# Kernel optimization log

Measured on AMD Instinct MI355X. Metric: run time of the kernel, lower is better.

The kernel has to match this reference:

```python
import jax, jax.numpy as jnp
import numpy as np

NUM_HEADS = 8
NUM_GROUPS = 32
EPS = 1e-5


def setup_inputs() -> dict:
    key = jax.random.key(0)
    ks = jax.random.split(key, 7)
    B, C, H, W = 8, 512, 32, 32
    x = jax.random.normal(ks[0], (B, C, H, W), dtype=jnp.float32)
    # GroupNorm affine params
    gn_w = jnp.ones((C,), dtype=jnp.float32)
    gn_b = jnp.zeros((C,), dtype=jnp.float32)
    # 1x1 conv == linear over channel dim; store squeezed weights (out, in)
    qkv_w = jax.random.normal(ks[1], (3 * C, C), dtype=jnp.float32) * (1.0 / np.sqrt(C))
    qkv_b = jnp.zeros((3 * C,), dtype=jnp.float32)
    proj_w = jax.random.normal(ks[2], (C, C), dtype=jnp.float32) * (1.0 / np.sqrt(C))
    proj_b = jnp.zeros((C,), dtype=jnp.float32)
    return {"x": x, "gn_w": gn_w, "gn_b": gn_b, "qkv_w": qkv_w,
            "qkv_b": qkv_b, "proj_w": proj_w, "proj_b": proj_b}


def reference(x, gn_w, gn_b, qkv_w, qkv_b, proj_w, proj_b):
    B, C, H, W = x.shape
    G = NUM_GROUPS
    hd = C // NUM_HEADS
    scale = hd ** -0.5
    # GroupNorm: normalize over (C//G, H, W) per group
    xg = x.reshape(B, G, C // G, H, W)
    mean = xg.mean(axis=(2, 3, 4), keepdims=True)
    var = xg.var(axis=(2, 3, 4), keepdims=True)
    xn = ((xg - mean) * jax.lax.rsqrt(var + EPS)).reshape(B, C, H, W)
    xn = xn * gn_w[None, :, None, None] + gn_b[None, :, None, None]
    # QKV 1x1 conv
    qkv = jnp.einsum('bchw,oc->bohw', xn, qkv_w) + qkv_b[None, :, None, None]
    # (B, 3, heads, head_dim, HW) -> (3, B, heads, HW, head_dim)
    qkv = qkv.reshape(B, 3, NUM_HEADS, hd, H * W).transpose(1, 0, 2, 4, 3)
    q, k, v = qkv[0], qkv[1], qkv[2]
    attn = jax.nn.softmax(jnp.einsum('bhqd,bhkd->bhqk', q, k) * scale, axis=-1)
    out = jnp.einsum('bhqk,bhkd->bhqd', attn, v)  # (B, heads, HW, hd)
    out = out.transpose(0, 1, 3, 2).reshape(B, C, H, W)
    out = jnp.einsum('bchw,oc->bohw', out, proj_w) + proj_b[None, :, None, None]
    return out + x
```

## Files before the change

kernel.cpp:

```cpp
#include <hip/hip_runtime.h>
#include <hip/hip_bf16.h>
#include <math.h>

typedef __bf16 bf16_t;
typedef __bf16 bf16x8 __attribute__((ext_vector_type(8)));
typedef __bf16 bf16x4 __attribute__((ext_vector_type(4)));
typedef float  f32x4  __attribute__((ext_vector_type(4)));
typedef short  short4v __attribute__((ext_vector_type(4)));

#define NB    8
#define NC    512
#define NHW   1024
#define NHEAD 8
#define NHD   64
#define NG    32
#define NCG   16
#define NO3   1536
#define KVB   64
#define NKT   16

__device__ __forceinline__ void lds_load16(bf16_t* lds, const bf16_t* g) {
  __builtin_amdgcn_global_load_lds(
      (__attribute__((address_space(1))) unsigned int*)(g),
      (__attribute__((address_space(3))) unsigned int*)(void*)(lds),
      16, 0, 0);
}

__device__ __forceinline__ f32x4 mfma16(bf16x4 a, bf16x4 b, f32x4 c) {
#if __has_builtin(__builtin_amdgcn_mfma_f32_16x16x16bf16_1k)
  return __builtin_amdgcn_mfma_f32_16x16x16bf16_1k(
      __builtin_bit_cast(short4v, a), __builtin_bit_cast(short4v, b), c, 0, 0, 0);
#else
  f32x4 d;
  asm("v_mfma_f32_16x16x16_bf16 %0, %1, %2, %3"
      : "=v"(d) : "v"(a), "v"(b), "v"(c));
  return d;
#endif
}

__device__ __forceinline__ float fexp2(float x) {
#if __has_builtin(__builtin_amdgcn_exp2f)
  return __builtin_amdgcn_exp2f(x);
#else
  return exp2f(x);
#endif
}

__global__ __launch_bounds__(256)
void gnw_kernel(const float* __restrict__ x, const float* __restrict__ gw,
                const float* __restrict__ gb, bf16_t* __restrict__ xn,
                const float* __restrict__ qw, const float* __restrict__ pw,
                bf16_t* __restrict__ qwb, bf16_t* __restrict__ pwb)
{
  const int bid = blockIdx.x;
  const int tid = threadIdx.x;

  if (bid >= NB * NG) {
    const int gid = (bid - NB * NG) * 256 + tid;
    const int n1 = NO3 * NC / 4;
    float4 v; bf16x4 o;
    if (gid < n1) {
      v = ((const float4*)qw)[gid];
      o[0] = (bf16_t)v.x; o[1] = (bf16_t)v.y; o[2] = (bf16_t)v.z; o[3] = (bf16_t)v.w;
      ((bf16x4*)qwb)[gid] = o;
    } else {
      int g2 = gid - n1;
      v = ((const float4*)pw)[g2];
      o[0] = (bf16_t)v.x; o[1] = (bf16_t)v.y; o[2] = (bf16_t)v.z; o[3] = (bf16_t)v.w;
      ((bf16x4*)pwb)[g2] = o;
    }
    return;
  }

  const int b = bid >> 5, g = bid & 31;
  const float* xp = x + ((size_t)b * NC + g * NCG) * NHW;
  const int wave = tid >> 6, lane = tid & 63;

  float4 v[16];
  const float4* xp4 = (const float4*)xp;
  float s1 = 0.f, s2 = 0.f;
  #pragma unroll
  for (int c = 0; c < 16; ++c) {
    v[c] = xp4[c * 256 + tid];
    s1 += v[c].x + v[c].y + v[c].z + v[c].w;
    s2 += v[c].x * v[c].x + v[c].y * v[c].y + v[c].z * v[c].z + v[c].w * v[c].w;
  }
  for (int off = 32; off > 0; off >>= 1) {
    s1 += __shfl_down(s1, off);
    s2 += __shfl_down(s2, off);
  }
  __shared__ float red[16];
  if (lane == 0) { red[wave] = s1; red[8 + wave] = s2; }
  __syncthreads();
  float tot1 = red[0] + red[1] + red[2] + red[3];
  float tot2 = red[8] + red[9] + red[10] + red[11];
  const float mean = tot1 * (1.0f / 16384.0f);
  const float var  = tot2 * (1.0f / 16384.0f) - mean * mean;
  const float rstd = rsqrtf(var + 1e-5f);

  float gam[NCG], bet[NCG];
  #pragma unroll
  for (int c = 0; c < NCG; ++c) {
    gam[c] = gw[g * NCG + c] * rstd;
    bet[c] = gb[g * NCG + c] - mean * gam[c];
  }
  bf16_t* op = xn + (size_t)b * NHW * NC + g * NCG;
  #pragma unroll
  for (int jj = 0; jj < 4; ++jj) {
    int s = 4 * tid + jj;
    __align__(16) bf16_t vals[NCG];
    #pragma unroll
    for (int c = 0; c < NCG; ++c) {
      float xv = (jj == 0) ? v[c].x : (jj == 1) ? v[c].y : (jj == 2) ? v[c].z : v[c].w;
      vals[c] = (bf16_t)(xv * gam[c] + bet[c]);
    }
    *(bf16x8*)(op + (size_t)s * NC)     = *(const bf16x8*)&vals[0];
    *(bf16x8*)(op + (size_t)s * NC + 8) = *(const bf16x8*)&vals[8];
  }
}

__global__ __launch_bounds__(256, 2)
void qkv_gemm(const bf16_t* __restrict__ xn, const bf16_t* __restrict__ w,
              const float* __restrict__ bias,
              bf16_t* __restrict__ qbuf, bf16_t* __restrict__ kbuf, bf16_t* __restrict__ vbuf)
{
  __shared__ __align__(16) char smem[65536];
  const int tid = threadIdx.x;
  const int wave = tid >> 6, lane = tid & 63;
  const int quad = lane >> 4, l16 = lane & 15;
  const int wm = wave >> 1, wn = wave & 1;
  const int bx = blockIdx.x, by = blockIdx.y, b = blockIdx.z;

  const bf16_t* Ap = xn + ((size_t)b * NHW + by * 128) * NC;
  const bf16_t* Bp = w + (size_t)bx * 128 * NC;

  auto stage = [&](int k0, int bufi) {
    bf16_t* sA = (bf16_t*)(smem + bufi * 32768);
    bf16_t* sB = (bf16_t*)(smem + bufi * 32768 + 16384);
    #pragma unroll
    for (int j = 0; j < 4; ++j) {
      int c = wave * 64 + j * 256 + lane;
      int row = c >> 3, ko = ((c ^ (c >> 3)) & 7) * 8;
      lds_load16(sA + (size_t)(wave * 64 + j * 256) * 8, Ap + (size_t)row * 512 + k0 + ko);
      lds_load16(sB + (size_t)(wave * 64 + j * 256) * 8, Bp + (size_t)row * 512 + k0 + ko);
    }
  };

  f32x4 acc[4][4] = {};
  stage(0, 0);
  __syncthreads();
  const int swr = (l16 & 7) << 4;
  for (int t = 0; t < 8; ++t) {
    const int cur = t & 1;
    if (t < 7) stage((t + 1) * 64, cur ^ 1);
    const char* sA = smem + cur * 32768;
    const char* sB = sA + 16384;
    #pragma unroll
    for (int kc = 0; kc < 2; ++kc) {
      bf16x8 af[4], bfr[4];
      #pragma unroll
      for (int mi = 0; mi < 4; ++mi)
        af[mi] = *(const bf16x8*)(sA + (wm * 64 + mi * 16 + l16) * 128 + ((kc * 64 + quad * 16) ^ swr));
      #pragma unroll
      for (int ni = 0; ni < 4; ++ni)
        bfr[ni] = *(const bf16x8*)(sB + (wn * 64 + ni * 16 + l16) * 128 + ((kc * 64 + quad * 16) ^ swr));
      #pragma unroll
      for (int mi = 0; mi < 4; ++mi)
        #pragma unroll
        for (int ni = 0; ni < 4; ++ni)
          acc[mi][ni] = __builtin_amdgcn_mfma_f32_16x16x32_bf16(af[mi], bfr[ni], acc[mi][ni], 0, 0, 0);
    }
    __syncthreads();
  }

  const int obase = bx * 128 + wn * 64;
  const int sbase = by * 128 + wm * 64;
  float bv[4];
  #pragma unroll
  for (int ni = 0; ni < 4; ++ni) bv[ni] = bias[obase + ni * 16 + l16];

  if (bx < 8) {
    const bool isq = (bx < 4);
    bf16_t* basep = isq ? qbuf : kbuf;
    const float scale = isq ? 0.18033688f : 1.0f;
    #pragma unroll
    for (int ni = 0; ni < 4; ++ni) {
      int o = obase + ni * 16 + l16;
      int hh = (o >> 6) & 7, dd = o & 63;
      bf16_t* dst = basep + ((size_t)(b * NHEAD + hh) * NHW) * NHD + dd;
      #pragma unroll
      for (int mi = 0; mi < 4; ++mi)
        #pragma unroll
        for (int r = 0; r < 4; ++r) {
          int s = sbase + mi * 16 + quad * 4 + r;
          dst[(size_t)s * NHD] = (bf16_t)((acc[mi][ni][r] + bv[ni]) * scale);
        }
    }
  } else {
    bf16_t* sC = (bf16_t*)smem;
    __syncthreads();
    #pragma unroll
    for (int ni = 0; ni < 4; ++ni)
      #pragma unroll
      for (int mi = 0; mi < 4; ++mi)
        #pragma unroll
        for (int r = 0; r < 4; ++r)
          sC[(wn * 64 + ni * 16 + l16) * 136 + wm * 64 + mi * 16 + quad * 4 + r] =
              (bf16_t)(acc[mi][ni][r] + bv[ni]);
    __syncthreads();
    int o_local = tid >> 1, shalf = (tid & 1) << 6;
    int ov = (bx - 8) * 128 + o_local;
    int hh = ov >> 6, dd = ov & 63;
    bf16_t* dst = vbuf + ((size_t)(b * NHEAD + hh) * NHD + dd) * NHW + by * 128 + shalf;
    #pragma unroll
    for (int jj = 0; jj < 8; ++jj)
      *(bf16x8*)(dst + jj * 8) = *(const bf16x8*)&sC[o_local * 136 + shalf + jj * 8];
  }
}

__global__ __launch_bounds__(256, 2)
void attn_kernel(const bf16_t* __restrict__ qbuf, const bf16_t* __restrict__ kbuf,
                 const bf16_t* __restrict__ vbuf, bf16_t* __restrict__ obuf)
{
  __shared__ __align__(16) char smem[32768];
  f32x4* mO = (f32x4*)smem;
  float* mM = (float*)(smem + 16384);
  float* mL = (float*)(smem + 17408);

  const int tid = threadIdx.x;
  const int wave = tid >> 6, lane = tid & 63;
  const int quad = lane >> 4, l16 = lane & 15;
  const int wl = wave & 1;
  const int wg = wave >> 1;
  const int idx = blockIdx.x;
  const int qt = idx >> 6, h = (idx >> 3) & 7, b = idx & 7;
  const size_t bh = (size_t)b * NHEAD + h;
  const bf16_t* qp = qbuf + (bh * NHW + qt * 64 + wl * 32) * NHD;
  const char* kp = (const char*)(kbuf + bh * NHW * NHD);
  const char* vp = (const char*)(vbuf + bh * NHD * NHW);

  const int r8 = lane >> 3;
  const int swc = (((lane & 7) << 4)) ^ (r8 << 4);

  bf16x8 qf[2][2];
  #pragma unroll
  for (int stile = 0; stile < 2; ++stile)
    #pragma unroll
    for (int kc = 0; kc < 2; ++kc)
      qf[stile][kc] = *(const bf16x8*)(qp + (size_t)(stile * 16 + l16) * NHD + kc * 32 + quad * 8);

  float m_i[2] = {-1e30f, -1e30f};
  float ll[2] = {0.f, 0.f};
  f32x4 oacc[4][2] = {};

  #pragma unroll
  for (int j = 0; j < 2; ++j) {
    int i = wave * 2 + j;
    const char* kg = kp + ((size_t)(i * 8 + r8) * NHD) * 2 + swc;
    lds_load16((bf16_t*)(smem + i * 1024), (const bf16_t*)kg);
    const char* vg = vp + ((size_t)(i * 8 + r8) * NHW) * 2 + swc;
    lds_load16((bf16_t*)(smem + 8192 + i * 1024), (const bf16_t*)vg);
  }
  __syncthreads();

  const int swr = (l16 & 7) << 4;

  for (int kt = 0; kt < NKT; ++kt) {
    const int cur = kt & 1;
    const char* Kb = smem + cur * 16384;
    const char* Vb = Kb + 8192;
    if (kt < NKT - 1) {
      char* Kn = smem + (cur ^ 1) * 16384;
      #pragma unroll
      for (int j = 0; j < 2; ++j) {
        int i = wave * 2 + j;
        const char* kg = kp + ((size_t)((kt + 1) * KVB + i * 8 + r8) * NHD) * 2 + swc;
        lds_load16((bf16_t*)(Kn + i * 1024), (const bf16_t*)kg);
        const char* vg = vp + ((size_t)(i * 8 + r8) * NHW + (kt + 1) * KVB) * 2 + swc;
        lds_load16((bf16_t*)(Kn + 8192 + i * 1024), (const bf16_t*)vg);
      }
    }

    f32x4 st[2][2];
    __builtin_amdgcn_s_setprio(1);
    #pragma unroll
    for (int mt = 0; mt < 2; ++mt) {
      const int mtg = wg * 2 + mt;
      const char* krow = Kb + (mtg * 16 + l16) * 128;
      bf16x8 ka0 = *(const bf16x8*)(krow + ((quad * 16) ^ swr));
      bf16x8 ka1 = *(const bf16x8*)(krow + ((64 + quad * 16) ^ swr));
      #pragma unroll
      for (int stile = 0; stile < 2; ++stile) {
        f32x4 z = {};
        z = __builtin_amdgcn_mfma_f32_16x16x32_bf16(ka0, qf[stile][0], z, 0, 0, 0);
        z = __builtin_amdgcn_mfma_f32_16x16x32_bf16(ka1, qf[stile][1], z, 0, 0, 0);
        st[stile][mt] = z;
      }
    }
    __builtin_amdgcn_s_setprio(0);

    #pragma unroll
    for (int stile = 0; stile < 2; ++stile) {
      float mx = st[stile][0][0];
      #pragma unroll
      for (int mt = 0; mt < 2; ++mt)
        #pragma unroll
        for (int r = 0; r < 4; ++r) mx = fmaxf(mx, st[stile][mt][r]);
      if (!__all(mx <= m_i[stile])) {
        mx = fmaxf(mx, __shfl_xor(mx, 16));
        mx = fmaxf(mx, __shfl_xor(mx, 32));
        float mnew = fmaxf(m_i[stile], mx);
        float alpha = fexp2(m_i[stile] - mnew);
        m_i[stile] = mnew;
        ll[stile] *= alpha;
        #pragma unroll
        for (int mi = 0; mi < 4; ++mi)
          #pragma unroll
          for (int r = 0; r < 4; ++r) oacc[mi][stile][r] *= alpha;
      }
      float rs = 0.f;
      #pragma unroll
      for (int mt = 0; mt < 2; ++mt)
        #pragma unroll
        for (int r = 0; r < 4; ++r) {
          float p = fexp2(st[stile][mt][r] - m_i[stile]);
          rs += p;
          st[stile][mt][r] = p;
        }
      ll[stile] += rs;
    }

    __builtin_amdgcn_s_setprio(1);
    #pragma unroll
    for (int mt = 0; mt < 2; ++mt) {
      const int mtg = wg * 2 + mt;
      bf16x4 pb[2];
      #pragma unroll
      for (int stile = 0; stile < 2; ++stile) {
        pb[stile][0] = (bf16_t)st[stile][mt][0];
        pb[stile][1] = (bf16_t)st[stile][mt][1];
        pb[stile][2] = (bf16_t)st[stile][mt][2];
        pb[stile][3] = (bf16_t)st[stile][mt][3];
      }
      #pragma unroll
      for (int mi = 0; mi < 4; ++mi) {
        const char* vrow = Vb + (mi * 16 + l16) * 128;
        bf16x4 va = *(const bf16x4*)(vrow + ((mtg * 32 + quad * 8) ^ swr));
        oacc[mi][0] = mfma16(va, pb[0], oacc[mi][0]);
        oacc[mi][1] = mfma16(va, pb[1], oacc[mi][1]);
      }
    }
    __builtin_amdgcn_s_setprio(0);
    __syncthreads();
  }

  float l_i[2];
  #pragma unroll
  for (int stile = 0; stile < 2; ++stile) {
    float rs = ll[stile];
    rs += __shfl_xor(rs, 16);
    rs += __shfl_xor(rs, 32);
    l_i[stile] = rs;
  }

  if (wg == 1) {
    #pragma unroll
    for (int stile = 0; stile < 2; ++stile) {
      mM[(wl * 2 + stile) * 64 + lane] = m_i[stile];
      mL[(wl * 2 + stile) * 64 + lane] = l_i[stile];
      #pragma unroll
      for (int mi = 0; mi < 4; ++mi)
        mO[((wl * 2 + stile) * 4 + mi) * 64 + lane] = oacc[mi][stile];
    }
  }
  __syncthreads();
  if (wg == 0) {
    #pragma unroll
    for (int stile = 0; stile < 2; ++stile) {
      float mB = mM[(wl * 2 + stile) * 64 + lane];
      float lB = mL[(wl * 2 + stile) * 64 + lane];
      float mS = fmaxf(m_i[stile], mB);
      float aA = fexp2(m_i[stile] - mS);
      float aB = fexp2(mB - mS);
      float inv = 1.0f / (l_i[stile] * aA + lB * aB);
      int s = qt * 64 + wl * 32 + stile * 16 + l16;
      bf16_t* orow = obuf + ((size_t)b * NHW + s) * NC + h * NHD;
      #pragma unroll
      for (int mi = 0; mi < 4; ++mi) {
        f32x4 oB = mO[((wl * 2 + stile) * 4 + mi) * 64 + lane];
        __align__(8) bf16_t o4[4];
        #pragma unroll
        for (int r = 0; r < 4; ++r)
          o4[r] = (bf16_t)((oacc[mi][stile][r] * aA + oB[r] * aB) * inv);
        *(bf16x4*)(orow + mi * 16 + quad * 4) = *(const bf16x4*)o4;
      }
    }
  }
}

__global__ __launch_bounds__(256, 2)
void proj_gemm(const bf16_t* __restrict__ ob, const bf16_t* __restrict__ w,
               const float* __restrict__ bias, const float* __restrict__ x,
               float* __restrict__ out)
{
  __shared__ __align__(16) char smem[49152];
  const int tid = threadIdx.x;
  const int wave = tid >> 6, lane = tid & 63;
  const int quad = lane >> 4, l16 = lane & 15;
  const int wm = wave & 1, wn = wave >> 1;
  const int bx = blockIdx.x, by = blockIdx.y, b = blockIdx.z;

  const bf16_t* Ap = w + (size_t)by * 64 * NC;
  const bf16_t* Bp = ob + ((size_t)b * NHW + bx * 128) * NC;

  auto stage = [&](int k0, int bufi) {
    bf16_t* sA = (bf16_t*)(smem + bufi * 24576);
    bf16_t* sB = (bf16_t*)(smem + bufi * 24576 + 8192);
    #pragma unroll
    for (int j = 0; j < 2; ++j) {
      int c = wave * 64 + j * 256 + lane;
      int row = c >> 3, ko = ((c ^ (c >> 3)) & 7) * 8;
      lds_load16(sA + (size_t)(wave * 64 + j * 256) * 8, Ap + (size_t)row * 512 + k0 + ko);
    }
    #pragma unroll
    for (int j = 0; j < 4; ++j) {
      int c = wave * 64 + j * 256 + lane;
      int row = c >> 3, ko = ((c ^ (c >> 3)) & 7) * 8;
      lds_load16(sB + (size_t)(wave * 64 + j * 256) * 8, Bp + (size_t)row * 512 + k0 + ko);
    }
  };

  f32x4 acc[2][4] = {};
  stage(0, 0);
  __syncthreads();
  const int swr = (l16 & 7) << 4;
  for (int t = 0; t < 8; ++t) {
    const int cur = t & 1;
    if (t < 7) stage((t + 1) * 64, cur ^ 1);
    const char* sA = smem + cur * 24576;
    const char* sB = sA + 8192;
    #pragma unroll
    for (int kc = 0; kc < 2; ++kc) {
      bf16x8 af[2], bfr[4];
      #pragma unroll
      for (int mi = 0; mi < 2; ++mi)
        af[mi] = *(const bf16x8*)(sA + (wm * 32 + mi * 16 + l16) * 128 + ((kc * 64 + quad * 16) ^ swr));
      #pragma unroll
      for (int ni = 0; ni < 4; ++ni)
        bfr[ni] = *(const bf16x8*)(sB + (wn * 64 + ni * 16 + l16) * 128 + ((kc * 64 + quad * 16) ^ swr));
      #pragma unroll
      for (int mi = 0; mi < 2; ++mi)
        #pragma unroll
        for (int ni = 0; ni < 4; ++ni)
          acc[mi][ni] = __builtin_amdgcn_mfma_f32_16x16x32_bf16(af[mi], bfr[ni], acc[mi][ni], 0, 0, 0);
    }
    __syncthreads();
  }

  const int cobase = by * 64 + wm * 32;
  const int sbase  = bx * 128 + wn * 64;
  #pragma unroll
  for (int mi = 0; mi < 2; ++mi)
    #pragma unroll
    for (int r = 0; r < 4; ++r) {
      int co = cobase + mi * 16 + quad * 4 + r;
      float pb = bias[co];
      const float* xrow = x + ((size_t)b * NC + co) * NHW;
      float* orow = out + ((size_t)b * NC + co) * NHW;
      #pragma unroll
      for (int ni = 0; ni < 4; ++ni) {
        int s = sbase + ni * 16 + l16;
        orow[s] = acc[mi][ni][r] + pb + xrow[s];
      }
    }
}

extern "C" void kernel_launch(void* const* d_in, const int* in_sizes, int n_in,
                              void* d_out, int out_size, void* d_ws, size_t ws_size,
                              hipStream_t stream)
{
  const float* x      = (const float*)d_in[0];
  const float* gn_w   = (const float*)d_in[1];
  const float* gn_b   = (const float*)d_in[2];
  const float* qkv_w  = (const float*)d_in[3];
  const float* qkv_b  = (const float*)d_in[4];
  const float* proj_w = (const float*)d_in[5];
  const float* proj_b = (const float*)d_in[6];
  float* out = (float*)d_out;

  char* ws = (char*)d_ws;
  bf16_t* xn   = (bf16_t*)(ws);
  bf16_t* qwb  = (bf16_t*)(ws + 8388608);
  bf16_t* pwb  = (bf16_t*)(ws + 9961472);
  bf16_t* qbuf = (bf16_t*)(ws + 10485760);
  bf16_t* kbuf = (bf16_t*)(ws + 18874368);
  bf16_t* vbuf = (bf16_t*)(ws + 27262976);
  bf16_t* obuf = xn;

  gnw_kernel<<<dim3(NB * NG + 1024), dim3(256), 0, stream>>>(
      x, gn_w, gn_b, xn, qkv_w, proj_w, qwb, pwb);
  qkv_gemm<<<dim3(12, 8, NB), dim3(256), 0, stream>>>(xn, qwb, qkv_b, qbuf, kbuf, vbuf);
  attn_kernel<<<dim3(1024), dim3(256), 0, stream>>>(qbuf, kbuf, vbuf, obuf);
  proj_gemm<<<dim3(8, 8, NB), dim3(256), 0, stream>>>(obuf, pwb, proj_b, x, out);
}
```

Baseline: 148.6 us.

## Double attention KV tile to 128 keys and remap QKV GEMM blocks per XCD

The attention kernel now stages 128 keys and values per iteration instead of 64, halving the number of loop iterations and barriers. The V tile uses a new swizzled layout with 256-byte rows. LDS use per block rises to 64 KB, which may lower occupancy. The QKV GEMM also moves to a 1D grid whose block index is remapped so that the 12 output-column tiles sharing one input row tile land on the same XCD, for better L2 reuse of the activation tile.

```diff
diff --git a/kernel.cpp b/kernel.cpp
--- a/kernel.cpp
+++ b/kernel.cpp
@@ -16,8 +16,8 @@
 #define NG    32
 #define NCG   16
 #define NO3   1536
-#define KVB   64
-#define NKT   16
+#define KVB   128
+#define NKT   8
 
 __device__ __forceinline__ void lds_load16(bf16_t* lds, const bf16_t* g) {
   __builtin_amdgcn_global_load_lds(
@@ -129,7 +129,11 @@
   const int wave = tid >> 6, lane = tid & 63;
   const int quad = lane >> 4, l16 = lane & 15;
   const int wm = wave >> 1, wn = wave & 1;
-  const int bx = blockIdx.x, by = blockIdx.y, b = blockIdx.z;
+  const int bid = blockIdx.x;
+  const int xcd = bid & 7, slot = bid >> 3;
+  const int pairIdx = xcd * 8 + slot / 12;
+  const int bx = slot % 12;
+  const int by = pairIdx & 7, b = pairIdx >> 3;
 
   const bf16_t* Ap = xn + ((size_t)b * NHW + by * 128) * NC;
   const bf16_t* Bp = w + (size_t)bx * 128 * NC;
@@ -222,7 +226,7 @@
 void attn_kernel(const bf16_t* __restrict__ qbuf, const bf16_t* __restrict__ kbuf,
                  const bf16_t* __restrict__ vbuf, bf16_t* __restrict__ obuf)
 {
-  __shared__ __align__(16) char smem[32768];
+  __shared__ __align__(16) char smem[65536];
   f32x4* mO = (f32x4*)smem;
   float* mM = (float*)(smem + 16384);
   float* mL = (float*)(smem + 17408);
@@ -253,39 +257,35 @@
   float ll[2] = {0.f, 0.f};
   f32x4 oacc[4][2] = {};
 
-  #pragma unroll
-  for (int j = 0; j < 2; ++j) {
-    int i = wave * 2 + j;
-    const char* kg = kp + ((size_t)(i * 8 + r8) * NHD) * 2 + swc;
-    lds_load16((bf16_t*)(smem + i * 1024), (const bf16_t*)kg);
-    const char* vg = vp + ((size_t)(i * 8 + r8) * NHW) * 2 + swc;
-    lds_load16((bf16_t*)(smem + 8192 + i * 1024), (const bf16_t*)vg);
-  }
+  auto stageKV = [&](int kt, char* buf) {
+    #pragma unroll
+    for (int j = 0; j < 4; ++j) {
+      int i = wave * 4 + j;
+      const char* kg = kp + ((size_t)(kt * KVB + i * 8 + r8) * NHD) * 2 + swc;
+      lds_load16((bf16_t*)(buf + i * 1024), (const bf16_t*)kg);
+      int dloc = i * 4 + (lane >> 4);
+      int vchunk = (lane & 15) ^ (((i & 1) << 2) | (lane >> 4));
+      const char* vg = vp + ((size_t)dloc * NHW + kt * KVB) * 2 + vchunk * 16;
+      lds_load16((bf16_t*)(buf + 16384 + i * 1024), (const bf16_t*)vg);
+    }
+  };
+
+  stageKV(0, smem);
   __syncthreads();
 
   const int swr = (l16 & 7) << 4;
 
   for (int kt = 0; kt < NKT; ++kt) {
     const int cur = kt & 1;
-    const char* Kb = smem + cur * 16384;
-    const char* Vb = Kb + 8192;
-    if (kt < NKT - 1) {
-      char* Kn = smem + (cur ^ 1) * 16384;
-      #pragma unroll
-      for (int j = 0; j < 2; ++j) {
-        int i = wave * 2 + j;
-        const char* kg = kp + ((size_t)((kt + 1) * KVB + i * 8 + r8) * NHD) * 2 + swc;
-        lds_load16((bf16_t*)(Kn + i * 1024), (const bf16_t*)kg);
-        const char* vg = vp + ((size_t)(i * 8 + r8) * NHW + (kt + 1) * KVB) * 2 + swc;
-        lds_load16((bf16_t*)(Kn + 8192 + i * 1024), (const bf16_t*)vg);
-      }
-    }
-
-    f32x4 st[2][2];
+    const char* Kb = smem + cur * 32768;
+    const char* Vb = Kb + 16384;
+    if (kt < NKT - 1) stageKV(kt + 1, smem + (cur ^ 1) * 32768);
+
+    f32x4 st[2][4];
     __builtin_amdgcn_s_setprio(1);
     #pragma unroll
-    for (int mt = 0; mt < 2; ++mt) {
-      const int mtg = wg * 2 + mt;
+    for (int mt = 0; mt < 4; ++mt) {
+      const int mtg = wg * 4 + mt;
       const char* krow = Kb + (mtg * 16 + l16) * 128;
       bf16x8 ka0 = *(const bf16x8*)(krow + ((quad * 16) ^ swr));
       bf16x8 ka1 = *(const bf16x8*)(krow + ((64 + quad * 16) ^ swr));
@@ -303,7 +303,7 @@
     for (int stile = 0; stile < 2; ++stile) {
       float mx = st[stile][0][0];
       #pragma unroll
-      for (int mt = 0; mt < 2; ++mt)
+      for (int mt = 0; mt < 4; ++mt)
         #pragma unroll
         for (int r = 0; r < 4; ++r) mx = fmaxf(mx, st[stile][mt][r]);
       if (!__all(mx <= m_i[stile])) {
@@ -320,7 +320,7 @@
       }
       float rs = 0.f;
       #pragma unroll
-      for (int mt = 0; mt < 2; ++mt)
+      for (int mt = 0; mt < 4; ++mt)
         #pragma unroll
         for (int r = 0; r < 4; ++r) {
           float p = fexp2(st[stile][mt][r] - m_i[stile]);
@@ -332,8 +332,8 @@
 
     __builtin_amdgcn_s_setprio(1);
     #pragma unroll
-    for (int mt = 0; mt < 2; ++mt) {
-      const int mtg = wg * 2 + mt;
+    for (int mt = 0; mt < 4; ++mt) {
+      const int mtg = wg * 4 + mt;
       bf16x4 pb[2];
       #pragma unroll
       for (int stile = 0; stile < 2; ++stile) {
@@ -342,10 +342,12 @@
         pb[stile][2] = (bf16_t)st[stile][mt][2];
         pb[stile][3] = (bf16_t)st[stile][mt][3];
       }
+      const int vch = (mtg << 1) | (quad >> 1);
+      const int vbo = (quad & 1) << 3;
       #pragma unroll
       for (int mi = 0; mi < 4; ++mi) {
-        const char* vrow = Vb + (mi * 16 + l16) * 128;
-        bf16x4 va = *(const bf16x4*)(vrow + ((mtg * 32 + quad * 8) ^ swr));
+        const char* vrow = Vb + (mi * 16 + l16) * 256;
+        bf16x4 va = *(const bf16x4*)(vrow + ((vch ^ (l16 & 7)) << 4) + vbo);
         oacc[mi][0] = mfma16(va, pb[0], oacc[mi][0]);
         oacc[mi][1] = mfma16(va, pb[1], oacc[mi][1]);
       }
@@ -499,7 +501,7 @@
 
   gnw_kernel<<<dim3(NB * NG + 1024), dim3(256), 0, stream>>>(
       x, gn_w, gn_b, xn, qkv_w, proj_w, qwb, pwb);
-  qkv_gemm<<<dim3(12, 8, NB), dim3(256), 0, stream>>>(xn, qwb, qkv_b, qbuf, kbuf, vbuf);
+  qkv_gemm<<<dim3(768), dim3(256), 0, stream>>>(xn, qwb, qkv_b, qbuf, kbuf, vbuf);
   attn_kernel<<<dim3(1024), dim3(256), 0, stream>>>(qbuf, kbuf, vbuf, obuf);
   proj_gemm<<<dim3(8, 8, NB), dim3(256), 0, stream>>>(obuf, pwb, proj_b, x, out);
 }
```

Result: slower. 153.4 us (+3.3%).
